# Kernel optimization log

Hardware: AMD Instinct MI355X
Metric: run time of the kernel (lower is better)

The kernel has to match this reference:

```python
import jax, jax.numpy as jnp
import numpy as np

# module hyperparameters (from init_kwargs ch_in=256, ch_out=256, hyper_in=128)
CH_IN, CH_OUT, HYPER_IN = 256, 256, 128
G = max(CH_OUT // 64, 1)            # num_gen = 4
G_IN, G_OUT = CH_IN // G, CH_OUT // G  # 64, 64
NW = G_OUT * G_IN * 9               # 36864 weights per group
NB = G_OUT                          # 64 biases per group
HD = int(max(HYPER_IN, NW + NB) * 0.25 + 0.5 * HYPER_IN) // G  # 2324


def setup_inputs() -> dict:
    key = jax.random.key(0)
    k0, k1, k2, k3 = jax.random.split(key, 4)
    B, H, W = 8, 64, 64
    image = jax.random.normal(k0, (B, CH_IN, H, W), jnp.float32)
    hyper = jax.random.normal(k1, (B, HYPER_IN), jnp.float32)
    # hypernetwork MLP params, stacked over the G generators
    W1 = jax.random.normal(k2, (G, HYPER_IN, HD), jnp.float32) * 0.05
    b1 = jnp.zeros((G, HD), jnp.float32)
    W2 = jax.random.normal(k3, (G, HD, NW + NB), jnp.float32) * 0.01
    b2 = jnp.zeros((G, NW + NB), jnp.float32)
    return {"image": image, "hyper": hyper, "W1": W1, "b1": b1, "W2": W2, "b2": b2}


def _hyperconv(image, hyper, W1, b1, W2, b2):
    B, C, H, W = image.shape
    # per-group hypernetwork: gened[g,b,:] = MLP_g(hyper[b])
    h = jax.nn.relu(jnp.einsum('bi,gid->gbd', hyper, W1) + b1[:, None, :])
    gened = jnp.einsum('gbd,gdo->gbo', h, W2) + b2[:, None, :]  # (G,B,NW+NB)
    w = gened[..., :NW].reshape(G, B, G_OUT, G_IN * 9)
    bias = gened[..., NW:].reshape(G, B, G_OUT)                 # (G,B,G_OUT)
    # 3x3 unfold with padding=1, channel ordering (c, kh, kw) like torch unfold
    xp = jnp.pad(image, ((0, 0), (0, 0), (1, 1), (1, 1)))
    patches = jnp.stack([xp[:, :, i:i + H, j:j + W]
                         for i in range(3) for j in range(3)], axis=2)  # (B,C,9,H,W)
    # block-diagonal weight => grouped dynamic conv: split channels into G groups
    patches = patches.reshape(B, G, G_IN * 9, H * W)
    out = jnp.einsum('gbok,bgkl->bgol', w, patches)             # (B,G,G_OUT,H*W)
    out = out.reshape(B, CH_OUT, H, W)
    bias = jnp.transpose(bias, (1, 0, 2)).reshape(B, CH_OUT, 1, 1)
    return out + bias


def reference(image, hyper, W1, b1, W2, b2):
    return _hyperconv(image, hyper, W1, b1, W2, b2)
```

## Files before the change

kernel.cpp:

```cpp
#include <hip/hip_runtime.h>

#define G 4
#define NBATCH 8
#define HIN 128
#define HD 2324
#define NW 36864
#define NO 36928
#define NO4 (NO / 4)
#define GIN 64
#define GOUT 64
#define HIMG 64
#define WIMG 64
#define CIN 256
#define DSPLIT 8
#define DCHUNK 292

typedef __attribute__((ext_vector_type(8))) short bf16x8;
typedef __attribute__((ext_vector_type(4))) float f32x4;

__device__ inline unsigned short bf16rne(float f) {
  union { float f; unsigned u; } x; x.f = f;
  unsigned r = (x.u + 0x7FFF + ((x.u >> 16) & 1)) >> 16;
  return (unsigned short)r;
}

__global__ __launch_bounds__(256) void k1_hyper_l1(
    const float* __restrict__ hyper, const float* __restrict__ W1,
    const float* __restrict__ b1, float* __restrict__ h_t) {
  int g = blockIdx.y;
  int d = blockIdx.x * 256 + threadIdx.x;
  if (d >= HD) return;
  const float* W1g = W1 + (size_t)g * HIN * HD + d;
  float bias = b1[g * HD + d];
  float acc[NBATCH];
#pragma unroll
  for (int b = 0; b < NBATCH; ++b) acc[b] = bias;
  for (int i = 0; i < HIN; ++i) {
    float wv = W1g[(size_t)i * HD];
#pragma unroll
    for (int b = 0; b < NBATCH; ++b)
      acc[b] = fmaf(hyper[b * HIN + i], wv, acc[b]);
  }
  float4* hp = (float4*)(h_t + ((size_t)g * HD + d) * 8);
  hp[0] = make_float4(fmaxf(acc[0], 0.f), fmaxf(acc[1], 0.f),
                      fmaxf(acc[2], 0.f), fmaxf(acc[3], 0.f));
  hp[1] = make_float4(fmaxf(acc[4], 0.f), fmaxf(acc[5], 0.f),
                      fmaxf(acc[6], 0.f), fmaxf(acc[7], 0.f));
}

#define FMA_D(wv, hoff)                                   \
  {                                                       \
    _Pragma("unroll")                                     \
    for (int b = 0; b < NBATCH; ++b) {                    \
      float hv = hh[(hoff) * 8 + b];                      \
      acc[b][0] = fmaf(hv, (wv)[0], acc[b][0]);           \
      acc[b][1] = fmaf(hv, (wv)[1], acc[b][1]);           \
      acc[b][2] = fmaf(hv, (wv)[2], acc[b][2]);           \
      acc[b][3] = fmaf(hv, (wv)[3], acc[b][3]);           \
    }                                                     \
  }

__global__ __launch_bounds__(256) void k2_hyper_l2(
    const float* __restrict__ h_t, const float* __restrict__ W2,
    float* __restrict__ partial) {
  int g = blockIdx.y, ds = blockIdx.z;
  int o4 = blockIdx.x * 256 + threadIdx.x;
  bool active = (o4 < NO4);
  if (!active) o4 = NO4 - 1;
  const f32x4* W2g = (const f32x4*)(W2 + (size_t)g * HD * NO) + o4;
  const float* hg = h_t + (size_t)g * HD * 8;
  int d0 = ds * DCHUNK;
  int d1 = d0 + DCHUNK; if (d1 > HD) d1 = HD;
  int nd = d1 - d0;

  f32x4 acc[NBATCH] = {};
  const size_t WS = NO4;
  const f32x4* Wp = W2g + (size_t)d0 * WS;
  f32x4 w0 = __builtin_nontemporal_load(Wp);
  f32x4 w1 = __builtin_nontemporal_load(Wp + WS);
  f32x4 w2 = __builtin_nontemporal_load(Wp + 2 * WS);
  f32x4 w3 = __builtin_nontemporal_load(Wp + 3 * WS);
  int dd = 0;
  for (; dd < nd - 4; dd += 4) {
    const f32x4* Wn = Wp + (size_t)(dd + 4) * WS;
    f32x4 n0 = __builtin_nontemporal_load(Wn);
    f32x4 n1 = __builtin_nontemporal_load(Wn + WS);
    f32x4 n2 = __builtin_nontemporal_load(Wn + 2 * WS);
    f32x4 n3 = __builtin_nontemporal_load(Wn + 3 * WS);
    const float* hh = hg + (size_t)(d0 + dd) * 8;
    FMA_D(w0, 0) FMA_D(w1, 1) FMA_D(w2, 2) FMA_D(w3, 3)
    w0 = n0; w1 = n1; w2 = n2; w3 = n3;
  }
  {
    const float* hh = hg + (size_t)(d0 + dd) * 8;
    FMA_D(w0, 0) FMA_D(w1, 1) FMA_D(w2, 2) FMA_D(w3, 3)
  }

  if (active) {
    f32x4* pout = (f32x4*)partial + ((size_t)ds * G * NBATCH + g * NBATCH) * NO4 + o4;
#pragma unroll
    for (int b = 0; b < NBATCH; ++b) pout[(size_t)b * NO4] = acc[b];
  }
}

__global__ __launch_bounds__(256) void k_wprep(
    const float* __restrict__ partial, const float* __restrict__ b2,
    short* __restrict__ wbf, float* __restrict__ bias_f) {
  int gb = blockIdx.y;
  int g = gb >> 3;
  int tid = threadIdx.x;
  if (blockIdx.x == 4) {
    if (tid < GOUT) {
      float s = b2[(size_t)g * NO + NW + tid];
#pragma unroll
      for (int ds = 0; ds < DSPLIT; ++ds)
        s += partial[((size_t)ds * G * NBATCH + gb) * NO + NW + tid];
      bias_f[gb * GOUT + tid] = s;
    }
    return;
  }
  __shared__ short lds[9216];
  int o0 = blockIdx.x * 16;
  const f32x4* b2p = (const f32x4*)(b2 + (size_t)g * NO) + o0 * 144;
  const f32x4* pbase = (const f32x4*)partial + (size_t)gb * NO4 + o0 * 144;
#pragma unroll
  for (int j = 0; j < 9; ++j) {
    int idx4 = tid + j * 256;
    f32x4 s = b2p[idx4];
#pragma unroll
    for (int ds = 0; ds < DSPLIT; ++ds) {
      f32x4 v = pbase[(size_t)ds * G * NBATCH * NO4 + idx4];
      s[0] += v[0]; s[1] += v[1]; s[2] += v[2]; s[3] += v[3];
    }
    int flbase = idx4 * 4;
#pragma unroll
    for (int e = 0; e < 4; ++e) {
      int fl = flbase + e;
      int ol = fl / 576;
      int rest = fl - ol * 576;
      int c = rest / 9, k = rest - c * 9;
      lds[k * 1024 + ol * 64 + c] = (short)bf16rne(s[e]);
    }
  }
  __syncthreads();
  short* wout = wbf + (size_t)gb * NW;
#pragma unroll
  for (int j = 0; j < 9; ++j) {
    int u = tid + j * 256;
    int k = u >> 8, rem = u & 255;
    ((uint2*)(wout + (size_t)k * 4096 + o0 * 64))[rem] = ((uint2*)lds)[u];
  }
}

__global__ __launch_bounds__(256) void k_iprep(
    const float* __restrict__ image, short* __restrict__ imgt) {
  int row = blockIdx.x;
  int g = blockIdx.y, b = blockIdx.z;
  int gb = g * NBATCH + b;
  int tid = threadIdx.x;
  short* rowp = imgt + ((size_t)gb * 66 + row) * 66 * 64;
  if (row == 0 || row == 65) {
    uint4 z = {0, 0, 0, 0};
    uint4* p = (uint4*)rowp;
#pragma unroll
    for (int i = 0; i < 3; ++i) {
      int idx = tid + i * 256;
      if (idx < 528) p[idx] = z;
    }
    return;
  }
  int y = row - 1;
  __shared__ float lds[64 * 65];
  int p = tid & 63, cg = tid >> 6;
#pragma unroll
  for (int i = 0; i < 16; ++i) {
    int c = cg * 16 + i;
    lds[p * 65 + c] = image[((size_t)b * CIN + g * GIN + c) * 4096 + y * 64 + p];
  }
  __syncthreads();
  int p2 = tid >> 2, cq = tid & 3;
  unsigned short tmp[16];
#pragma unroll
  for (int i = 0; i < 16; ++i) tmp[i] = bf16rne(lds[p2 * 65 + cq * 16 + i]);
  short* dst = rowp + (p2 + 1) * 64 + cq * 16;
  *(uint4*)dst = *(uint4*)&tmp[0];
  *(uint4*)(dst + 8) = *(uint4*)&tmp[8];
  if (tid < 16) {
    ((uint2*)rowp)[tid] = make_uint2(0, 0);
  } else if (tid < 32) {
    ((uint2*)(rowp + 65 * 64))[tid - 16] = make_uint2(0, 0);
  }
}

__global__ __launch_bounds__(256) void k3_mfma(
    const short* __restrict__ wbf, const short* __restrict__ imgt,
    const float* __restrict__ bias_f, float* __restrict__ outbuf) {
  int g = blockIdx.y, b = blockIdx.z;
  int gb = g * NBATCH + b;
  int ygrp = blockIdx.x >> 1, ms = blockIdx.x & 1;
  int tid = threadIdx.x;
  int w = tid >> 6, l = tid & 63;
  int y = ygrp * 4 + w;
  int lo = l & 15;
  int hi = l >> 4;

  const short* wgb = wbf + (size_t)gb * 9 * 4096 + (size_t)ms * 32 * 64;
  const short* ibase = imgt + (((size_t)gb * 66 + y) * 66 + lo) * 64 + hi * 8;

  f32x4 acc[2][4] = {};
  bf16x8 a0[2], b0[4], a1[2], b1[4];

#define LA(dst, ks) { int s_ = (ks) >> 1, h_ = (ks) & 1;                      \
    const short* p_ = wgb + (size_t)s_ * 4096 + lo * 64 + h_ * 32 + hi * 8;   \
    _Pragma("unroll") for (int m_ = 0; m_ < 2; ++m_)                          \
      dst[m_] = *(const bf16x8*)(p_ + m_ * 1024); }
#define LB(dst, ks) { int s_ = (ks) >> 1, h_ = (ks) & 1;                      \
    int dy_ = s_ / 3, dx_ = s_ - 3 * dy_;                                     \
    const short* p_ = ibase + ((size_t)dy_ * 66 + dx_) * 64 + h_ * 32;        \
    _Pragma("unroll") for (int n_ = 0; n_ < 4; ++n_)                          \
      dst[n_] = *(const bf16x8*)(p_ + n_ * 1024); }
#define MM(aa, bb) { _Pragma("unroll") for (int m_ = 0; m_ < 2; ++m_)         \
    _Pragma("unroll") for (int n_ = 0; n_ < 4; ++n_)                          \
      acc[m_][n_] = __builtin_amdgcn_mfma_f32_16x16x32_bf16(                  \
          aa[m_], bb[n_], acc[m_][n_], 0, 0, 0); }

  LA(a0, 0) LB(b0, 0)
#pragma unroll
  for (int it = 0; it < 9; ++it) {
    LA(a1, 2 * it + 1) LB(b1, 2 * it + 1)
    MM(a0, b0)
    if (it < 8) { LA(a0, 2 * it + 2) LB(b0, 2 * it + 2) }
    MM(a1, b1)
  }

  float* op = outbuf + ((size_t)b * CIN + g * GOUT) * 4096 + y * 64;
#pragma unroll
  for (int m = 0; m < 2; ++m)
#pragma unroll
    for (int j = 0; j < 4; ++j) {
      int o = ms * 32 + m * 16 + hi * 4 + j;
      float bias = bias_f[gb * 64 + o];
#pragma unroll
      for (int n = 0; n < 4; ++n)
        op[(size_t)o * 4096 + n * 16 + lo] = acc[m][n][j] + bias;
    }
#undef LA
#undef LB
#undef MM
}

extern "C" void kernel_launch(void* const* d_in, const int* in_sizes, int n_in,
                              void* d_out, int out_size, void* d_ws, size_t ws_size,
                              hipStream_t stream) {
  const float* image = (const float*)d_in[0];
  const float* hyper = (const float*)d_in[1];
  const float* W1    = (const float*)d_in[2];
  const float* b1    = (const float*)d_in[3];
  const float* W2    = (const float*)d_in[4];
  const float* b2    = (const float*)d_in[5];
  float* out = (float*)d_out;

  float* h_t     = (float*)d_ws;
  float* bias_f  = h_t + (size_t)G * HD * 8;
  float* partial = bias_f + G * NBATCH * GOUT;
  short* wbf     = (short*)(partial + (size_t)DSPLIT * G * NBATCH * NO);
  short* imgt    = wbf + (size_t)G * NBATCH * 9 * 4096;

  k_iprep<<<dim3(66, G, NBATCH), 256, 0, stream>>>(image, imgt);
  k1_hyper_l1<<<dim3((HD + 255) / 256, G), 256, 0, stream>>>(hyper, W1, b1, h_t);
  k2_hyper_l2<<<dim3((NO4 + 255) / 256, G, DSPLIT), 256, 0, stream>>>(h_t, W2, partial);
  k_wprep<<<dim3(5, G * NBATCH), 256, 0, stream>>>(partial, b2, wbf, bias_f);
  k3_mfma<<<dim3(32, G, NBATCH), 256, 0, stream>>>(wbf, imgt, bias_f, out);
}
```

Measured before the change: 323.4 us.

## Fuse hyper layer-1 into image prep, widen MFMA tile, pad LDS

Moves the first hypernetwork layer into extra blocks of the image-prep kernel, which removes one kernel launch. The MFMA conv kernel now has each block compute all 64 output channels instead of 32, so the B image fragments are reused across more MFMAs. It also switches to a flat 1D grid with interleaved group/batch ordering. The weight-prep LDS buffer is padded per kernel tap (stride 1056) to reduce bank conflicts. The larger tile doubles the accumulator registers and halves the block count to 512, which may lower occupancy.

```diff
diff --git a/kernel.cpp b/kernel.cpp
--- a/kernel.cpp
+++ b/kernel.cpp
@@ -22,30 +22,6 @@
   union { float f; unsigned u; } x; x.f = f;
   unsigned r = (x.u + 0x7FFF + ((x.u >> 16) & 1)) >> 16;
   return (unsigned short)r;
-}
-
-__global__ __launch_bounds__(256) void k1_hyper_l1(
-    const float* __restrict__ hyper, const float* __restrict__ W1,
-    const float* __restrict__ b1, float* __restrict__ h_t) {
-  int g = blockIdx.y;
-  int d = blockIdx.x * 256 + threadIdx.x;
-  if (d >= HD) return;
-  const float* W1g = W1 + (size_t)g * HIN * HD + d;
-  float bias = b1[g * HD + d];
-  float acc[NBATCH];
-#pragma unroll
-  for (int b = 0; b < NBATCH; ++b) acc[b] = bias;
-  for (int i = 0; i < HIN; ++i) {
-    float wv = W1g[(size_t)i * HD];
-#pragma unroll
-    for (int b = 0; b < NBATCH; ++b)
-      acc[b] = fmaf(hyper[b * HIN + i], wv, acc[b]);
-  }
-  float4* hp = (float4*)(h_t + ((size_t)g * HD + d) * 8);
-  hp[0] = make_float4(fmaxf(acc[0], 0.f), fmaxf(acc[1], 0.f),
-                      fmaxf(acc[2], 0.f), fmaxf(acc[3], 0.f));
-  hp[1] = make_float4(fmaxf(acc[4], 0.f), fmaxf(acc[5], 0.f),
-                      fmaxf(acc[6], 0.f), fmaxf(acc[7], 0.f));
 }
 
 #define FMA_D(wv, hoff)                                   \
@@ -119,7 +95,7 @@
     }
     return;
   }
-  __shared__ short lds[9216];
+  __shared__ short lds[9 * 1056];
   int o0 = blockIdx.x * 16;
   const f32x4* b2p = (const f32x4*)(b2 + (size_t)g * NO) + o0 * 144;
   const f32x4* pbase = (const f32x4*)partial + (size_t)gb * NO4 + o0 * 144;
@@ -139,7 +115,7 @@
       int ol = fl / 576;
       int rest = fl - ol * 576;
       int c = rest / 9, k = rest - c * 9;
-      lds[k * 1024 + ol * 64 + c] = (short)bf16rne(s[e]);
+      lds[k * 1056 + ol * 64 + c] = (short)bf16rne(s[e]);
     }
   }
   __syncthreads();
@@ -148,16 +124,41 @@
   for (int j = 0; j < 9; ++j) {
     int u = tid + j * 256;
     int k = u >> 8, rem = u & 255;
-    ((uint2*)(wout + (size_t)k * 4096 + o0 * 64))[rem] = ((uint2*)lds)[u];
+    ((uint2*)(wout + (size_t)k * 4096 + o0 * 64))[rem] =
+        ((uint2*)(lds + k * 1056))[rem];
   }
 }
 
 __global__ __launch_bounds__(256) void k_iprep(
-    const float* __restrict__ image, short* __restrict__ imgt) {
+    const float* __restrict__ image, short* __restrict__ imgt,
+    const float* __restrict__ hyper, const float* __restrict__ W1,
+    const float* __restrict__ b1, float* __restrict__ h_t) {
   int row = blockIdx.x;
   int g = blockIdx.y, b = blockIdx.z;
+  int tid = threadIdx.x;
+  if (row >= 66) {
+    if (b != 0) return;
+    int d = (row - 66) * 256 + tid;
+    if (d >= HD) return;
+    const float* W1g = W1 + (size_t)g * HIN * HD + d;
+    float bias = b1[g * HD + d];
+    float acc[NBATCH];
+#pragma unroll
+    for (int bb = 0; bb < NBATCH; ++bb) acc[bb] = bias;
+    for (int i = 0; i < HIN; ++i) {
+      float wv = W1g[(size_t)i * HD];
+#pragma unroll
+      for (int bb = 0; bb < NBATCH; ++bb)
+        acc[bb] = fmaf(hyper[bb * HIN + i], wv, acc[bb]);
+    }
+    float4* hp = (float4*)(h_t + ((size_t)g * HD + d) * 8);
+    hp[0] = make_float4(fmaxf(acc[0], 0.f), fmaxf(acc[1], 0.f),
+                        fmaxf(acc[2], 0.f), fmaxf(acc[3], 0.f));
+    hp[1] = make_float4(fmaxf(acc[4], 0.f), fmaxf(acc[5], 0.f),
+                        fmaxf(acc[6], 0.f), fmaxf(acc[7], 0.f));
+    return;
+  }
   int gb = g * NBATCH + b;
-  int tid = threadIdx.x;
   short* rowp = imgt + ((size_t)gb * 66 + row) * 66 * 64;
   if (row == 0 || row == 65) {
     uint4 z = {0, 0, 0, 0};
@@ -195,31 +196,32 @@
 __global__ __launch_bounds__(256) void k3_mfma(
     const short* __restrict__ wbf, const short* __restrict__ imgt,
     const float* __restrict__ bias_f, float* __restrict__ outbuf) {
-  int g = blockIdx.y, b = blockIdx.z;
-  int gb = g * NBATCH + b;
-  int ygrp = blockIdx.x >> 1, ms = blockIdx.x & 1;
+  int lin = blockIdx.x;
+  int gb = (lin & 7) * 4 + ((lin >> 3) & 3);
+  int ygrp = lin >> 5;
+  int g = gb >> 3, b = gb & 7;
   int tid = threadIdx.x;
   int w = tid >> 6, l = tid & 63;
   int y = ygrp * 4 + w;
   int lo = l & 15;
   int hi = l >> 4;
 
-  const short* wgb = wbf + (size_t)gb * 9 * 4096 + (size_t)ms * 32 * 64;
+  const short* wgb = wbf + (size_t)gb * 9 * 4096;
   const short* ibase = imgt + (((size_t)gb * 66 + y) * 66 + lo) * 64 + hi * 8;
 
-  f32x4 acc[2][4] = {};
-  bf16x8 a0[2], b0[4], a1[2], b1[4];
+  f32x4 acc[4][4] = {};
+  bf16x8 a0[4], b0[4], a1[4], b1[4];
 
 #define LA(dst, ks) { int s_ = (ks) >> 1, h_ = (ks) & 1;                      \
     const short* p_ = wgb + (size_t)s_ * 4096 + lo * 64 + h_ * 32 + hi * 8;   \
-    _Pragma("unroll") for (int m_ = 0; m_ < 2; ++m_)                          \
+    _Pragma("unroll") for (int m_ = 0; m_ < 4; ++m_)                          \
       dst[m_] = *(const bf16x8*)(p_ + m_ * 1024); }
 #define LB(dst, ks) { int s_ = (ks) >> 1, h_ = (ks) & 1;                      \
     int dy_ = s_ / 3, dx_ = s_ - 3 * dy_;                                     \
     const short* p_ = ibase + ((size_t)dy_ * 66 + dx_) * 64 + h_ * 32;        \
     _Pragma("unroll") for (int n_ = 0; n_ < 4; ++n_)                          \
       dst[n_] = *(const bf16x8*)(p_ + n_ * 1024); }
-#define MM(aa, bb) { _Pragma("unroll") for (int m_ = 0; m_ < 2; ++m_)         \
+#define MM(aa, bb) { _Pragma("unroll") for (int m_ = 0; m_ < 4; ++m_)         \
     _Pragma("unroll") for (int n_ = 0; n_ < 4; ++n_)                          \
       acc[m_][n_] = __builtin_amdgcn_mfma_f32_16x16x32_bf16(                  \
           aa[m_], bb[n_], acc[m_][n_], 0, 0, 0); }
@@ -235,10 +237,10 @@
 
   float* op = outbuf + ((size_t)b * CIN + g * GOUT) * 4096 + y * 64;
 #pragma unroll
-  for (int m = 0; m < 2; ++m)
+  for (int m = 0; m < 4; ++m)
 #pragma unroll
     for (int j = 0; j < 4; ++j) {
-      int o = ms * 32 + m * 16 + hi * 4 + j;
+      int o = m * 16 + hi * 4 + j;
       float bias = bias_f[gb * 64 + o];
 #pragma unroll
       for (int n = 0; n < 4; ++n)
@@ -266,9 +268,9 @@
   short* wbf     = (short*)(partial + (size_t)DSPLIT * G * NBATCH * NO);
   short* imgt    = wbf + (size_t)G * NBATCH * 9 * 4096;
 
-  k_iprep<<<dim3(66, G, NBATCH), 256, 0, stream>>>(image, imgt);
-  k1_hyper_l1<<<dim3((HD + 255) / 256, G), 256, 0, stream>>>(hyper, W1, b1, h_t);
+  k_iprep<<<dim3(76, G, NBATCH), 256, 0, stream>>>(image, imgt,
+                                                   hyper, W1, b1, h_t);
   k2_hyper_l2<<<dim3((NO4 + 255) / 256, G, DSPLIT), 256, 0, stream>>>(h_t, W2, partial);
   k_wprep<<<dim3(5, G * NBATCH), 256, 0, stream>>>(partial, b2, wbf, bias_f);
-  k3_mfma<<<dim3(32, G, NBATCH), 256, 0, stream>>>(wbf, imgt, bias_f, out);
-}
+  k3_mfma<<<dim3(512), 256, 0, stream>>>(wbf, imgt, bias_f, out);
+}
```

Result: faster. 300.1 us (-7.2%).
